# Performance work log

Hardware: AMD Instinct MI355X
Metric: run time of the kernel (lower is better)

## Reference

```python
import jax, jax.numpy as jnp
import numpy as np
from jax.scipy.linalg import solve_triangular

OMEGA = 1.5  # params_fix['omega']
BS, N, MAXITER = 512, 256, 200
RTOL = 1e-6


def setup_inputs() -> dict:
    key = jax.random.key(0)
    k1, k2, k3 = jax.random.split(key, 3)
    # diagonally dominant A so SOR converges
    A = jax.random.normal(k1, (BS, N, N), jnp.float32) + N * jnp.eye(N, dtype=jnp.float32)
    b = jax.random.normal(k2, (BS, N), jnp.float32)
    x_sol = jnp.linalg.solve(A, b[..., None])[..., 0]
    theta = jax.random.normal(k3, (BS, N), jnp.float32)  # initial iterate x0
    rtol = jnp.full((BS,), RTOL, jnp.float32)
    return {"A": A, "b": b, "x_sol": x_sol, "theta": theta, "rtol": rtol, "maxiter": MAXITER}


def reference(A, b, x_sol, theta, rtol, maxiter):
    bs, n, _ = A.shape
    b = b.reshape(bs, n, 1)
    x0 = theta.reshape(bs, n, 1)
    xs = x_sol.reshape(bs, n, 1)

    diag = jnp.diagonal(A, axis1=1, axis2=2)          # [bs, n]
    D = jnp.eye(n, dtype=A.dtype) * diag[:, :, None]  # diag_embed
    L = jnp.tril(A, -1)
    U = jnp.triu(A, 1)

    omega = jnp.asarray(OMEGA, A.dtype)
    G1 = D + omega * L                      # lower triangular, [bs, n, n]
    G2 = omega * U + (omega - 1.0) * D
    G = solve_triangular(G1, -G2, lower=True)        # iteration matrix
    f = solve_triangular(G1, omega * b, lower=True)  # affine term

    err0 = jnp.linalg.norm(xs - x0, axis=(1, 2))     # [bs]
    xtol = jnp.linalg.norm(xs, axis=(1, 2)) * rtol   # [bs]

    def step(carry, _):
        x, err, done = carry
        # global stopping criterion: while any(err > xtol)
        done = jnp.logical_or(done, jnp.logical_not(jnp.any(err > xtol)))
        x_new = jnp.where(done, x, G @ x + f)
        err_new = jnp.where(done, err, jnp.linalg.norm(xs - x_new, axis=(1, 2)))
        hist = jnp.where(done, jnp.zeros_like(err), err_new)  # unwritten slots stay 0
        return (x_new, err_new, done), hist

    init = (x0, err0, jnp.asarray(False))
    _, hist = jax.lax.scan(step, init, None, length=maxiter)  # hist: [maxiter, bs]
    return jnp.concatenate([err0[:, None], hist.T], axis=1)   # [bs, maxiter+1]
```

## Files before the change

### kernel.cpp

```cpp
#include <hip/hip_runtime.h>
#include <math.h>

#define BS 512
#define NN 256
#define RB 16
#define OMEGA_F 1.5f

__global__ __launch_bounds__(1024, 4) void sor_fused(
    const float* __restrict__ A,
    const float* __restrict__ xs,
    const float* __restrict__ x0,
    const float* __restrict__ rtol,
    const int* __restrict__ maxiter_p,
    float* __restrict__ out)
{
    const int b   = blockIdx.x;
    const int tid = threadIdx.x;
    const int t   = tid & 255;
    const int q   = tid >> 8;
    const int qU  = __builtin_amdgcn_readfirstlane(q);
    const int w   = tid >> 6;
    const int u   = tid & 63;
    const float* __restrict__ Ab = A + (size_t)b * NN * NN;

    __shared__ __align__(16) char smem[65536];
    float (*ldsA)[NN]     = (float (*)[NN])(smem);
    float (*acc2)[RB][NN] = (float (*)[RB][NN])(smem + 16384);
    float (*xbuf)[NN]     = (float (*)[NN])(smem + 49152);
    float (*ldsX)[NN]     = (float (*)[NN])(smem);
    float* rs             = (float*)(smem + 16384);
    float* e              = (float*)(smem);
    float4 (*buf)[64]     = (float4 (*)[64])(smem + 1024);
    float* errs_p         = (float*)(smem + 17408);

    const int mi = *maxiter_p;
    float* __restrict__ outb = out + (size_t)b * (mi + 1);

    float ev = 0.f;
    if (q == 0) {
        const float xsv = xs[b * NN + t];
        ev = xsv - x0[b * NN + t];
        float s1 = ev * ev, s2 = xsv * xsv;
        #pragma unroll
        for (int off = 32; off > 0; off >>= 1) {
            s1 += __shfl_down(s1, off);
            s2 += __shfl_down(s2, off);
        }
        if ((t & 63) == 0) { rs[t >> 6] = s1; rs[4 + (t >> 6)] = s2; }
    }
    __syncthreads();
    const float err0 = sqrtf(rs[0] + rs[1] + rs[2] + rs[3]);
    const float xtol = sqrtf(rs[4] + rs[5] + rs[6] + rs[7]) * rtol[b];
    if (tid == 0) outb[0] = err0;

    float g[4][RB];
    for (int KB = 0; KB < NN / RB; ++KB) {
        const int r0 = KB * RB;
        __syncthreads();
        {
            const int rr = tid >> 6;
            const int c  = (tid & 63) << 2;
            *(float4*)&ldsA[rr][c] = *(const float4*)&Ab[(size_t)(r0 + rr) * NN + c];
        }
        __syncthreads();

        float acc[RB];
        #pragma unroll
        for (int rr = 0; rr < RB; ++rr) acc[rr] = 0.f;
        #pragma unroll
        for (int m = 0; m < 4; ++m) {
            const int kbj = 4 * m + qU;
            if (kbj < KB) {
                const int j0 = kbj * RB;
                #pragma unroll
                for (int jw = 0; jw < 4; ++jw) {
                    const float g0 = g[m][4 * jw + 0];
                    const float g1 = g[m][4 * jw + 1];
                    const float g2 = g[m][4 * jw + 2];
                    const float g3 = g[m][4 * jw + 3];
                    #pragma unroll
                    for (int hc = 0; hc < 4; ++hc) {
                        float4 a_[4];
                        #pragma unroll
                        for (int h = 0; h < 4; ++h)
                            a_[h] = *(const float4*)&Ab[(size_t)(r0 + 4 * hc + h) * NN + j0 + 4 * jw];
                        #pragma unroll
                        for (int h = 0; h < 4; ++h)
                            acc[4 * hc + h] += a_[h].x * g0 + a_[h].y * g1
                                             + a_[h].z * g2 + a_[h].w * g3;
                    }
                }
            }
        }

        if (q < 2) {
            #pragma unroll
            for (int rr = 0; rr < RB; ++rr) acc2[q][rr][t] = acc[rr];
        }
        __syncthreads();
        if (q >= 2) {
            #pragma unroll
            for (int rr = 0; rr < RB; ++rr) acc2[q - 2][rr][t] += acc[rr];
        }
        __syncthreads();

        if (q == 0) {
            float s_[RB];
            #pragma unroll
            for (int rr = 0; rr < RB; ++rr)
                s_[rr] = acc2[0][rr][t] + acc2[1][rr][t];
            #pragma unroll
            for (int rr = 0; rr < RB; ++rr) {
                const int r = r0 + rr;
                const float a_rt = ldsA[rr][t];
                const float brt  = (t > r) ? (-OMEGA_F) * a_rt
                                 : ((t == r) ? (1.0f - OMEGA_F) * a_rt : 0.0f);
                const float diag = ldsA[rr][r];
                const float val  = (brt - OMEGA_F * s_[rr]) / diag;
                xbuf[rr][t] = val;
                #pragma unroll
                for (int rr2 = rr + 1; rr2 < RB; ++rr2)
                    s_[rr2] += ldsA[rr2][r] * val;
            }
        }
        __syncthreads();
        #pragma unroll
        for (int m = 0; m < 4; ++m) {
            if ((KB >> 2) == m && (KB & 3) == q) {
                #pragma unroll
                for (int rr = 0; rr < RB; ++rr) g[m][rr] = xbuf[rr][t];
            }
        }
    }

    float4 gi[16];
    #pragma unroll
    for (int R = 0; R < 4; ++R) {
        __syncthreads();
        #pragma unroll
        for (int rr = 0; rr < RB; ++rr) {
            const int lr = q * RB + rr;
            ldsX[lr][(t + lr) & 255] = g[R][rr];
        }
        __syncthreads();
        if ((u >> 4) == R) {
            #pragma unroll
            for (int jj = 0; jj < 16; ++jj) {
                const int tcol = 16 * w + jj;
                float vx[4];
                #pragma unroll
                for (int c = 0; c < 4; ++c) {
                    const int lr = 4 * (u & 15) + c;
                    vx[c] = ldsX[lr][(tcol + lr) & 255];
                }
                gi[jj] = make_float4(vx[0], vx[1], vx[2], vx[3]);
            }
        }
    }
    __syncthreads();

    if (tid < NN) e[tid] = ev;
    __syncthreads();

    float err = err0;
    int s = 1;
    for (; s <= mi; ++s) {
        if (!(err > xtol)) break;
        float4 acc4 = make_float4(0.f, 0.f, 0.f, 0.f);
        #pragma unroll
        for (int m = 0; m < 4; ++m) {
            const float4 evv = *(const float4*)&e[16 * w + 4 * m];
            acc4.x += gi[4*m+0].x*evv.x + gi[4*m+1].x*evv.y + gi[4*m+2].x*evv.z + gi[4*m+3].x*evv.w;
            acc4.y += gi[4*m+0].y*evv.x + gi[4*m+1].y*evv.y + gi[4*m+2].y*evv.z + gi[4*m+3].y*evv.w;
            acc4.z += gi[4*m+0].z*evv.x + gi[4*m+1].z*evv.y + gi[4*m+2].z*evv.z + gi[4*m+3].z*evv.w;
            acc4.w += gi[4*m+0].w*evv.x + gi[4*m+1].w*evv.y + gi[4*m+2].w*evv.z + gi[4*m+3].w*evv.w;
        }
        buf[w][u] = acc4;
        __syncthreads();
        float4 p;
        if (w < 4) {
            const float4 p1 = buf[w + 4][u], p2 = buf[w + 8][u], p3 = buf[w + 12][u];
            p.x = acc4.x + p1.x + p2.x + p3.x;
            p.y = acc4.y + p1.y + p2.y + p3.y;
            p.z = acc4.z + p1.z + p2.z + p3.z;
            p.w = acc4.w + p1.w + p2.w + p3.w;
            if (w) buf[w][u] = p;
        }
        __syncthreads();
        if (w == 0) {
            const float4 b1 = buf[1][u], b2 = buf[2][u], b3 = buf[3][u];
            float4 r;
            r.x = p.x + b1.x + b2.x + b3.x;
            r.y = p.y + b1.y + b2.y + b3.y;
            r.z = p.z + b1.z + b2.z + b3.z;
            r.w = p.w + b1.w + b2.w + b3.w;
            *(float4*)&e[4 * u] = r;
            float loc = r.x * r.x + r.y * r.y + r.z * r.z + r.w * r.w;
            #pragma unroll
            for (int off = 32; off > 0; off >>= 1) loc += __shfl_down(loc, off);
            if (u == 0) {
                const float er = sqrtf(loc);
                *errs_p = er;
                outb[s] = er;
            }
        }
        __syncthreads();
        err = *errs_p;
    }
    for (int idx = s + tid; idx <= mi; idx += 1024) outb[idx] = 0.f;
}

extern "C" void kernel_launch(void* const* d_in, const int* in_sizes, int n_in,
                              void* d_out, int out_size, void* d_ws, size_t ws_size,
                              hipStream_t stream) {
    const float* A     = (const float*)d_in[0];
    const float* xs    = (const float*)d_in[2];
    const float* theta = (const float*)d_in[3];
    const float* rtol  = (const float*)d_in[4];
    const int*   mi    = (const int*)d_in[5];
    float* out = (float*)d_out;

    sor_fused<<<dim3(BS), dim3(1024), 0, stream>>>(
        A, xs, theta, rtol, mi, out);
}
```

Before: 698.6 us.

## Halve block to 512 threads and restructure G distribution and iteration reduction

The workgroup shrinks from 1024 to 512 threads, with each thread holding twice as many G columns in registers (g[8][RB], gi[4][8]). The build phase now uses a two-way cross-wave reduction instead of four-way, which drops one barrier per row block. The iteration loop partitions the columns per wave and reduces partials through LDS into 256 outputs, so the final norm is computed by every thread without an extra broadcast barrier. The aim is fewer barriers and less LDS reduction traffic per iteration, at the cost of higher register pressure and less parallelism per block.

```diff
diff --git a/kernel.cpp b/kernel.cpp
--- a/kernel.cpp
+++ b/kernel.cpp
@@ -6,7 +6,7 @@
 #define RB 16
 #define OMEGA_F 1.5f
 
-__global__ __launch_bounds__(1024, 4) void sor_fused(
+__global__ __launch_bounds__(512, 1) void sor_fused(
     const float* __restrict__ A,
     const float* __restrict__ xs,
     const float* __restrict__ x0,
@@ -19,19 +19,19 @@
     const int t   = tid & 255;
     const int q   = tid >> 8;
     const int qU  = __builtin_amdgcn_readfirstlane(q);
-    const int w   = tid >> 6;
+    const int w   = __builtin_amdgcn_readfirstlane(tid >> 6);
     const int u   = tid & 63;
     const float* __restrict__ Ab = A + (size_t)b * NN * NN;
 
     __shared__ __align__(16) char smem[65536];
-    float (*ldsA)[NN]     = (float (*)[NN])(smem);
-    float (*acc2)[RB][NN] = (float (*)[RB][NN])(smem + 16384);
-    float (*xbuf)[NN]     = (float (*)[NN])(smem + 49152);
-    float (*ldsX)[NN]     = (float (*)[NN])(smem);
-    float* rs             = (float*)(smem + 16384);
-    float* e              = (float*)(smem);
-    float4 (*buf)[64]     = (float4 (*)[64])(smem + 1024);
-    float* errs_p         = (float*)(smem + 17408);
+    float (*ldsA)[NN]    = (float (*)[NN])(smem);
+    float (*acc2)[NN]    = (float (*)[NN])(smem + 16384);
+    float (*xbuf)[NN]    = (float (*)[NN])(smem + 32768);
+    float (*ldsX)[NN]    = (float (*)[NN])(smem);
+    float* rs            = (float*)(smem + 16384);
+    float* e             = (float*)(smem);
+    float (*pbuf)[4][64] = (float (*)[4][64])(smem + 1024);
+    float* nrm           = (float*)(smem + 1024 + 8192);
 
     const int mi = *maxiter_p;
     float* __restrict__ outb = out + (size_t)b * (mi + 1);
@@ -53,14 +53,15 @@
     const float xtol = sqrtf(rs[4] + rs[5] + rs[6] + rs[7]) * rtol[b];
     if (tid == 0) outb[0] = err0;
 
-    float g[4][RB];
+    float g[8][RB];
     for (int KB = 0; KB < NN / RB; ++KB) {
         const int r0 = KB * RB;
         __syncthreads();
-        {
-            const int rr = tid >> 6;
-            const int c  = (tid & 63) << 2;
-            *(float4*)&ldsA[rr][c] = *(const float4*)&Ab[(size_t)(r0 + rr) * NN + c];
+        #pragma unroll
+        for (int i = 0; i < 2; ++i) {
+            const int lin = tid + 512 * i;
+            const int rr = lin >> 6, c4 = (lin & 63) << 2;
+            *(float4*)&ldsA[rr][c4] = *(const float4*)&Ab[(size_t)(r0 + rr) * NN + c4];
         }
         __syncthreads();
 
@@ -68,10 +69,10 @@
         #pragma unroll
         for (int rr = 0; rr < RB; ++rr) acc[rr] = 0.f;
         #pragma unroll
-        for (int m = 0; m < 4; ++m) {
-            const int kbj = 4 * m + qU;
-            if (kbj < KB) {
-                const int j0 = kbj * RB;
+        for (int m = 0; m < 8; ++m) {
+            const int kb = 2 * m + qU;
+            if (kb < KB) {
+                const int j0 = kb * RB;
                 #pragma unroll
                 for (int jw = 0; jw < 4; ++jw) {
                     const float g0 = g[m][4 * jw + 0];
@@ -92,23 +93,15 @@
                 }
             }
         }
-
-        if (q < 2) {
-            #pragma unroll
-            for (int rr = 0; rr < RB; ++rr) acc2[q][rr][t] = acc[rr];
-        }
-        __syncthreads();
-        if (q >= 2) {
-            #pragma unroll
-            for (int rr = 0; rr < RB; ++rr) acc2[q - 2][rr][t] += acc[rr];
-        }
-        __syncthreads();
-
+        if (q == 1) {
+            #pragma unroll
+            for (int rr = 0; rr < RB; ++rr) acc2[rr][t] = acc[rr];
+        }
+        __syncthreads();
         if (q == 0) {
             float s_[RB];
             #pragma unroll
-            for (int rr = 0; rr < RB; ++rr)
-                s_[rr] = acc2[0][rr][t] + acc2[1][rr][t];
+            for (int rr = 0; rr < RB; ++rr) s_[rr] = acc[rr] + acc2[rr][t];
             #pragma unroll
             for (int rr = 0; rr < RB; ++rr) {
                 const int r = r0 + rr;
@@ -124,37 +117,30 @@
             }
         }
         __syncthreads();
-        #pragma unroll
-        for (int m = 0; m < 4; ++m) {
-            if ((KB >> 2) == m && (KB & 3) == q) {
-                #pragma unroll
-                for (int rr = 0; rr < RB; ++rr) g[m][rr] = xbuf[rr][t];
-            }
-        }
-    }
-
-    float4 gi[16];
+        if ((KB & 1) == q) {
+            const int m = KB >> 1;
+            #pragma unroll
+            for (int rr = 0; rr < RB; ++rr) g[m][rr] = xbuf[rr][t];
+        }
+    }
+
+    float4 gi[4][8];
     #pragma unroll
     for (int R = 0; R < 4; ++R) {
         __syncthreads();
         #pragma unroll
-        for (int rr = 0; rr < RB; ++rr) {
-            const int lr = q * RB + rr;
-            ldsX[lr][(t + lr) & 255] = g[R][rr];
-        }
-        __syncthreads();
-        if ((u >> 4) == R) {
-            #pragma unroll
-            for (int jj = 0; jj < 16; ++jj) {
-                const int tcol = 16 * w + jj;
-                float vx[4];
-                #pragma unroll
-                for (int c = 0; c < 4; ++c) {
-                    const int lr = 4 * (u & 15) + c;
-                    vx[c] = ldsX[lr][(tcol + lr) & 255];
-                }
-                gi[jj] = make_float4(vx[0], vx[1], vx[2], vx[3]);
+        for (int i = 0; i < 2; ++i) {
+            #pragma unroll
+            for (int rr = 0; rr < RB; ++rr) {
+                const int lr = (2 * i + q) * RB + rr;
+                ldsX[lr][(t + 4 * lr) & 255] = g[2 * R + i][rr];
             }
+        }
+        __syncthreads();
+        #pragma unroll
+        for (int jj4 = 0; jj4 < 8; ++jj4) {
+            const int c = 32 * w + 4 * jj4;
+            gi[R][jj4] = *(const float4*)&ldsX[u][(c + 4 * u) & 255];
         }
     }
     __syncthreads();
@@ -162,52 +148,41 @@
     if (tid < NN) e[tid] = ev;
     __syncthreads();
 
+    const float4* __restrict__ e4 = (const float4*)e;
     float err = err0;
     int s = 1;
     for (; s <= mi; ++s) {
         if (!(err > xtol)) break;
-        float4 acc4 = make_float4(0.f, 0.f, 0.f, 0.f);
-        #pragma unroll
-        for (int m = 0; m < 4; ++m) {
-            const float4 evv = *(const float4*)&e[16 * w + 4 * m];
-            acc4.x += gi[4*m+0].x*evv.x + gi[4*m+1].x*evv.y + gi[4*m+2].x*evv.z + gi[4*m+3].x*evv.w;
-            acc4.y += gi[4*m+0].y*evv.x + gi[4*m+1].y*evv.y + gi[4*m+2].y*evv.z + gi[4*m+3].y*evv.w;
-            acc4.z += gi[4*m+0].z*evv.x + gi[4*m+1].z*evv.y + gi[4*m+2].z*evv.z + gi[4*m+3].z*evv.w;
-            acc4.w += gi[4*m+0].w*evv.x + gi[4*m+1].w*evv.y + gi[4*m+2].w*evv.z + gi[4*m+3].w*evv.w;
-        }
-        buf[w][u] = acc4;
-        __syncthreads();
-        float4 p;
-        if (w < 4) {
-            const float4 p1 = buf[w + 4][u], p2 = buf[w + 8][u], p3 = buf[w + 12][u];
-            p.x = acc4.x + p1.x + p2.x + p3.x;
-            p.y = acc4.y + p1.y + p2.y + p3.y;
-            p.z = acc4.z + p1.z + p2.z + p3.z;
-            p.w = acc4.w + p1.w + p2.w + p3.w;
-            if (w) buf[w][u] = p;
-        }
-        __syncthreads();
-        if (w == 0) {
-            const float4 b1 = buf[1][u], b2 = buf[2][u], b3 = buf[3][u];
-            float4 r;
-            r.x = p.x + b1.x + b2.x + b3.x;
-            r.y = p.y + b1.y + b2.y + b3.y;
-            r.z = p.z + b1.z + b2.z + b3.z;
-            r.w = p.w + b1.w + b2.w + b3.w;
-            *(float4*)&e[4 * u] = r;
-            float loc = r.x * r.x + r.y * r.y + r.z * r.z + r.w * r.w;
+        float a0 = 0.f, a1 = 0.f, a2 = 0.f, a3 = 0.f;
+        #pragma unroll
+        for (int jj4 = 0; jj4 < 8; ++jj4) {
+            const float4 ev4 = e4[8 * w + jj4];
+            a0 += gi[0][jj4].x*ev4.x + gi[0][jj4].y*ev4.y + gi[0][jj4].z*ev4.z + gi[0][jj4].w*ev4.w;
+            a1 += gi[1][jj4].x*ev4.x + gi[1][jj4].y*ev4.y + gi[1][jj4].z*ev4.z + gi[1][jj4].w*ev4.w;
+            a2 += gi[2][jj4].x*ev4.x + gi[2][jj4].y*ev4.y + gi[2][jj4].z*ev4.z + gi[2][jj4].w*ev4.w;
+            a3 += gi[3][jj4].x*ev4.x + gi[3][jj4].y*ev4.y + gi[3][jj4].z*ev4.z + gi[3][jj4].w*ev4.w;
+        }
+        pbuf[w][0][u] = a0;
+        pbuf[w][1][u] = a1;
+        pbuf[w][2][u] = a2;
+        pbuf[w][3][u] = a3;
+        __syncthreads();
+        if (tid < NN) {
+            const int kk = tid >> 6, uu = tid & 63;
+            float sum = 0.f;
+            #pragma unroll
+            for (int w2 = 0; w2 < 8; ++w2) sum += pbuf[w2][kk][uu];
+            e[tid] = sum;
+            float loc = sum * sum;
             #pragma unroll
             for (int off = 32; off > 0; off >>= 1) loc += __shfl_down(loc, off);
-            if (u == 0) {
-                const float er = sqrtf(loc);
-                *errs_p = er;
-                outb[s] = er;
-            }
-        }
-        __syncthreads();
-        err = *errs_p;
-    }
-    for (int idx = s + tid; idx <= mi; idx += 1024) outb[idx] = 0.f;
+            if (uu == 0) nrm[kk] = loc;
+        }
+        __syncthreads();
+        err = sqrtf(nrm[0] + nrm[1] + nrm[2] + nrm[3]);
+        if (tid == 0) outb[s] = err;
+    }
+    for (int idx = s + tid; idx <= mi; idx += 512) outb[idx] = 0.f;
 }
 
 extern "C" void kernel_launch(void* const* d_in, const int* in_sizes, int n_in,
@@ -220,6 +195,6 @@
     const int*   mi    = (const int*)d_in[5];
     float* out = (float*)d_out;
 
-    sor_fused<<<dim3(BS), dim3(1024), 0, stream>>>(
+    sor_fused<<<dim3(BS), dim3(512), 0, stream>>>(
         A, xs, theta, rtol, mi, out);
 }
```

After: 609.9 us. 12.7% less time.
